# Kernel tuning notes

Hardware: AMD Instinct MI355X
Metric: run time of the kernel (lower is better)

The kernel has to match this reference:

```python
import jax, jax.numpy as jnp
import numpy as np

TEXT = 226          # text_seq_length
D = 1024            # model / inner dim
HEADS = 16
HD = D // HEADS     # 64
F = 13              # latent frames
FH, FW = 8, 12      # feature h/w = H/8/2, W/8/2
ST = F * FH * FW    # 1248 spatial tokens
S = TEXT + ST       # 1474 full sequence
NEG = -1e9


def sdpa(q, k, v, bias=None):
    # q:[b,h,Q,d] k,v:[b,h,K,d]; math path of F.scaled_dot_product_attention
    scale = 1.0 / jnp.sqrt(jnp.asarray(q.shape[-1], q.dtype))
    s = jnp.einsum('bhqd,bhkd->bhqk', q, k) * scale
    if bias is not None:
        s = s + bias
    p = jax.nn.softmax(s, axis=-1)
    return jnp.einsum('bhqk,bhkd->bhqd', p, v)


def setup_inputs() -> dict:
    key = jax.random.key(0)
    ks = jax.random.split(key, 11)
    w = 0.02
    return {
        'hidden_states': jax.random.normal(ks[0], (2, ST, D), jnp.float32),
        'encoder_hidden_states': jax.random.normal(ks[1], (2, TEXT, D), jnp.float32),
        'mask': jax.random.randint(ks[2], (F, 1, FH, FW), 0, 2),  # masks_for_attn (binary)
        'wq': jax.random.normal(ks[3], (D, D), jnp.float32) * w,
        'bq': jnp.zeros((D,), jnp.float32),
        'wk': jax.random.normal(ks[4], (D, D), jnp.float32) * w,
        'bk': jnp.zeros((D,), jnp.float32),
        'wv': jax.random.normal(ks[5], (D, D), jnp.float32) * w,
        'bv': jnp.zeros((D,), jnp.float32),
        'wo': jax.random.normal(ks[6], (D, D), jnp.float32) * w,
        'bo': jnp.zeros((D,), jnp.float32),
    }


def reference(hidden_states, encoder_hidden_states, mask, wq, bq, wk, bk, wv, bv, wo, bo):
    B = hidden_states.shape[0]  # 2: [cond, uncond]
    x = jnp.concatenate([encoder_hidden_states, hidden_states], axis=1)  # [2,S,D]

    def proj(w, b):
        y = x @ w + b                                   # [2,S,D]
        return y.reshape(B, S, HEADS, HD).transpose(0, 2, 1, 3)  # [2,H,S,hd]

    q = proj(wq, bq)
    k = proj(wk, bk)
    v = proj(wv, bv)

    # chunk into cond / uncond (source)
    key_cond, source_key = k[0:1], k[1:2]
    value_cond, source_value = v[0:1], v[1:2]

    # spatio-temporal source K/V (drop text tokens)
    st_source_key = source_key[:, :, TEXT:, :]    # [1,H,ST,hd]
    st_source_value = source_value[:, :, TEXT:, :]

    # 'masked' selective attention: the torch code gathers, per frame, the
    # source tokens where masks_for_attn > 0 and concatenates them after
    # key_cond. Softmax over a gathered subset == softmax over the full
    # appended set with -inf bias on unselected positions (identical math).
    sel = (mask[:, 0] > 0).reshape(-1)            # [ST] frame-major f,h,w order
    append_bias = jnp.where(sel, 0.0, NEG).astype(q.dtype)
    bias = jnp.concatenate([jnp.zeros((S,), q.dtype), append_bias])[None, None, None, :]  # [1,1,1,S+ST]

    st_key_cond = jnp.concatenate([key_cond, st_source_key], axis=2)      # [1,H,S+ST,hd]
    st_value_cond = jnp.concatenate([value_cond, st_source_value], axis=2)

    text_q = q[0:1, :, :TEXT, :]
    st_q = q[0:1, :, TEXT:, :]

    # extend_st_for_text_keys=True: text queries also attend to extended keys
    text_hs = sdpa(text_q, st_key_cond, st_value_cond, bias)  # [1,H,TEXT,hd]
    st_hs = sdpa(st_q, st_key_cond, st_value_cond, bias)      # [1,H,ST,hd]
    cond_hs = jnp.concatenate([text_hs, st_hs], axis=2)       # [1,H,S,hd]

    uncond_hs = sdpa(q[1:2], k[1:2], v[1:2])                  # [1,H,S,hd]

    hs = jnp.concatenate([cond_hs, uncond_hs], axis=0)        # [2,H,S,hd]
    hs = hs.transpose(0, 2, 1, 3).reshape(B, S, D)
    out = hs @ wo + bo                                        # to_out[0]; to_out[1] dropout is identity in eval

    return out[:, TEXT:, :], out[:, :TEXT, :]                 # (hidden_states, encoder_hidden_states)
```

## Files before the change

kernel.cpp:

```cpp
#include <hip/hip_runtime.h>
#include <hip/hip_bf16.h>

#define TEXT_N 226
#define D_N    1024
#define HEADS_N 16
#define HD_N   64
#define ST_N   1248
#define S_N    1474
#define L0_N   2722
#define NT_C   43
#define NT_U   24
#define BC_N   (NT_C*64)
#define SP_N   1536
#define MB_N   24
#define KB_N   16
#define NEGB2  (-1.442695e9f)
#define SCALE2 (0.125f * 1.44269504f)

typedef __hip_bfloat16 bf16_t;
typedef short s16x8 __attribute__((ext_vector_type(8)));
typedef short s16x4 __attribute__((ext_vector_type(4)));
typedef float f32x4 __attribute__((ext_vector_type(4)));

__device__ __forceinline__ f32x4 mfma16(s16x8 a, s16x8 b, f32x4 c) {
    return __builtin_amdgcn_mfma_f32_16x16x32_bf16(a, b, c, 0, 0, 0);
}

typedef __attribute__((address_space(1))) const unsigned int gu32;
typedef __attribute__((address_space(3))) unsigned int lu32;
__device__ __forceinline__ void glds16(const void* g, void* l) {
    __builtin_amdgcn_global_load_lds((gu32*)g, (lu32*)l, 16, 0, 0);
}

__device__ __forceinline__ short f2bs(float x) {
    unsigned u = __float_as_uint(x);
    u += 0x7FFF + ((u >> 16) & 1);
    return (short)(u >> 16);
}
__device__ __forceinline__ unsigned pk2(float a, float b) {
    float2 f; f.x = a; f.y = b;
    __hip_bfloat162 h = __float22bfloat162_rn(f);
    return *(unsigned*)&h;
}
__device__ __forceinline__ int swz(int r, int c) {
    return r * 64 + ((((c >> 3) ^ (r & 7)) << 3) | (c & 7));
}

__global__ __launch_bounds__(256) void prep(
    const float* __restrict__ hid, const float* __restrict__ enc,
    const int* __restrict__ mask,
    const float* __restrict__ wq, const float* __restrict__ wk,
    const float* __restrict__ wv, const float* __restrict__ wo,
    bf16_t* __restrict__ wimg, bf16_t* __restrict__ xb,
    float* __restrict__ biasc, float* __restrict__ biasu) {
    __shared__ float Lw[64 * 129];
    const int b = blockIdx.x, t = threadIdx.x;
    if (b < 512) {
        const int wid = b >> 7, nblk = (b >> 4) & 7, kb = b & 15;
        const float* w = (wid == 0) ? wq : (wid == 1) ? wk : (wid == 2) ? wv : wo;
        const int k0 = kb * 64, n0 = nblk * 128;
#pragma unroll
        for (int i = 0; i < 8; i++) {
            int idx = t + i * 256;
            int kr = idx >> 5, c4 = (idx & 31) * 4;
            float4 v = *(const float4*)(w + (size_t)(k0 + kr) * D_N + n0 + c4);
            Lw[kr * 129 + c4 + 0] = v.x; Lw[kr * 129 + c4 + 1] = v.y;
            Lw[kr * 129 + c4 + 2] = v.z; Lw[kr * 129 + c4 + 3] = v.w;
        }
        __syncthreads();
        bf16_t* dst = wimg + (((size_t)wid * 8 + nblk) * 16 + kb) * 8192;
#pragma unroll
        for (int i = 0; i < 4; i++) {
            int u = t + i * 256;
            int r = u >> 3, p = u & 7;
            int ul = p ^ (r & 7);
            s16x8 o;
#pragma unroll
            for (int e = 0; e < 8; e++)
                o[e] = f2bs(Lw[(ul * 8 + e) * 129 + r]);
            *(s16x8*)(dst + r * 64 + p * 8) = o;
        }
    } else if (b < 896) {
        const int tile = b - 512;
        const int mblk = tile >> 4, kb = tile & 15;
        bf16_t* dst = xb + (size_t)tile * 8192;
#pragma unroll
        for (int i = 0; i < 4; i++) {
            int u = t + i * 256;
            int r = u >> 3, p = u & 7;
            int m = mblk * 128 + r;
            int bb = m >= SP_N; int s = m - bb * SP_N;
            if (s >= S_N) continue;
            const float* src = (s < TEXT_N)
                ? (enc + (size_t)(bb * TEXT_N + s) * D_N)
                : (hid + (size_t)(bb * ST_N + (s - TEXT_N)) * D_N);
            int k = kb * 64 + (p ^ (r & 7)) * 8;
            float4 f0 = *(const float4*)(src + k);
            float4 f1 = *(const float4*)(src + k + 4);
            s16x8 o;
            o[0]=f2bs(f0.x); o[1]=f2bs(f0.y); o[2]=f2bs(f0.z); o[3]=f2bs(f0.w);
            o[4]=f2bs(f1.x); o[5]=f2bs(f1.y); o[6]=f2bs(f1.z); o[7]=f2bs(f1.w);
            *(s16x8*)(dst + r * 64 + p * 8) = o;
        }
    } else {
        int j = (b - 896) * 256 + t;
        if (j < BC_N) {
            float v = -8.f;
            if (j >= L0_N) v = NEGB2;
            else if (j >= S_N) v = (mask[j - S_N] > 0) ? -8.f : NEGB2;
            biasc[j] = v;
        }
        int j2 = j - BC_N;
        if (j2 >= 0 && j2 < SP_N) biasu[j2] = (j2 < S_N) ? -8.f : NEGB2;
    }
}

__global__ __launch_bounds__(256) void qkv_proj(
    const bf16_t* __restrict__ xb, const bf16_t* __restrict__ wimg,
    const float* __restrict__ bq, const float* __restrict__ bk, const float* __restrict__ bv,
    bf16_t* __restrict__ Q, bf16_t* __restrict__ Kc, bf16_t* __restrict__ Ku,
    bf16_t* __restrict__ Vc, bf16_t* __restrict__ Vu) {
    __shared__ __align__(16) bf16_t As[4096];
    __shared__ __align__(16) bf16_t Bs[8192];
    const int z = blockIdx.z;
    const float* bias = (z == 0) ? bq : (z == 1) ? bk : bv;
    const int nblk = blockIdx.x, mblk = blockIdx.y;
    const int m0 = mblk * 64;
    const int mt = mblk >> 1, rowOff = (mblk & 1) * 64;
    const int t = threadIdx.x, wave = t >> 6, lane = t & 63, ln = lane & 15, qd = lane >> 4;
    const bf16_t* Ai = xb + ((size_t)mt * KB_N) * 8192 + rowOff * 64;
    const bf16_t* Bi = wimg + ((size_t)z * 8 + nblk) * KB_N * 8192;

    f32x4 acc[8];
    const f32x4 z4 = {0.f, 0.f, 0.f, 0.f};
#pragma unroll
    for (int ni = 0; ni < 8; ni++) acc[ni] = z4;

    for (int kb = 0; kb < KB_N; kb++) {
        const bf16_t* at = Ai + (size_t)kb * 8192;
        const bf16_t* bt = Bi + (size_t)kb * 8192;
#pragma unroll
        for (int i = 0; i < 2; i++)
            glds16(at + (t + i * 256) * 8, As + (t + i * 256) * 8);
#pragma unroll
        for (int i = 0; i < 4; i++)
            glds16(bt + (t + i * 256) * 8, Bs + (t + i * 256) * 8);
        __syncthreads();
#pragma unroll
        for (int kk = 0; kk < 2; kk++) {
            const int po = (((kk * 4 + qd) ^ (ln & 7)) << 3);
            s16x8 af = *(const s16x8*)(As + (wave * 16 + ln) * 64 + po);
#pragma unroll
            for (int ni = 0; ni < 8; ni++) {
                s16x8 bfr = *(const s16x8*)(Bs + (ni * 16 + ln) * 64 + po);
                acc[ni] = mfma16(af, bfr, acc[ni]);
            }
        }
        __syncthreads();
    }

    const int b = m0 >= SP_N;
    const int sbase = m0 - b * SP_N + wave * 16 + qd * 4;
#pragma unroll
    for (int ni = 0; ni < 8; ni++) {
        int n = nblk * 128 + ni * 16 + ln;
        float bn = bias[n];
        int h = n >> 6, d = n & 63;
        int s = sbase;
        if (s >= S_N) continue;
        if (z == 2) {
            s16x4 pk;
#pragma unroll
            for (int r = 0; r < 4; r++) pk[r] = f2bs(acc[ni][r] + bn);
            bool full = (s + 3 < S_N);
            if (!b) {
                if (full) {
                    *(s16x4*)(Vc + ((size_t)h * NT_C + (s >> 6)) * 4096 + swz(d, s & 63)) = pk;
                } else {
                    for (int r = 0; r < 4; r++)
                        if (s + r < S_N)
                            *(short*)&Vc[((size_t)h * NT_C + ((s + r) >> 6)) * 4096 + swz(d, (s + r) & 63)] = pk[r];
                }
            } else {
                if (full) {
                    *(s16x4*)(Vu + ((size_t)h * NT_U + (s >> 6)) * 4096 + swz(d, s & 63)) = pk;
                    if (s >= TEXT_N) {
                        int j = s + 1248;
                        *(s16x4*)(Vc + ((size_t)h * NT_C + (j >> 6)) * 4096 + swz(d, j & 63)) = pk;
                    } else if (s + 3 >= TEXT_N) {
                        for (int r = 0; r < 4; r++)
                            if (s + r >= TEXT_N) {
                                int j = s + r + 1248;
                                *(short*)&Vc[((size_t)h * NT_C + (j >> 6)) * 4096 + swz(d, j & 63)] = pk[r];
                            }
                    }
                } else {
                    for (int r = 0; r < 4; r++)
                        if (s + r < S_N) {
                            *(short*)&Vu[((size_t)h * NT_U + ((s + r) >> 6)) * 4096 + swz(d, (s + r) & 63)] = pk[r];
                            if (s + r >= TEXT_N) {
                                int j = s + r + 1248;
                                *(short*)&Vc[((size_t)h * NT_C + (j >> 6)) * 4096 + swz(d, j & 63)] = pk[r];
                            }
                        }
                }
            }
        } else {
#pragma unroll
            for (int r = 0; r < 4; r++) {
                int sr = s + r;
                if (sr >= S_N) continue;
                short v = f2bs(acc[ni][r] + bn);
                if (z == 0) {
                    *(short*)&Q[((size_t)(b * HEADS_N + h) * SP_N + sr) * HD_N + d] = v;
                } else {
                    if (!b) {
                        *(short*)&Kc[((size_t)h * NT_C + (sr >> 6)) * 4096 + swz(sr & 63, d)] = v;
                    } else {
                        *(short*)&Ku[((size_t)h * NT_U + (sr >> 6)) * 4096 + swz(sr & 63, d)] = v;
                        if (sr >= TEXT_N) {
                            int j = sr + 1248;
                            *(short*)&Kc[((size_t)h * NT_C + (j >> 6)) * 4096 + swz(j & 63, d)] = v;
                        }
                    }
                }
            }
        }
    }
}

__global__ __launch_bounds__(256) void attn_k(
    const bf16_t* __restrict__ Q, const bf16_t* __restrict__ Kc, const bf16_t* __restrict__ Ku,
    const bf16_t* __restrict__ Vc, const bf16_t* __restrict__ Vu,
    const float* __restrict__ biasc, const float* __restrict__ biasu,
    bf16_t* __restrict__ hs) {
    __shared__ __align__(16) bf16_t Ks[4096];
    __shared__ __align__(16) bf16_t Vs[4096];
    __shared__ __align__(16) bf16_t Ps[4][1024];
    __shared__ __align__(16) float  bsL[BC_N];
    const int cs = blockIdx.z, h = blockIdx.y, q0 = blockIdx.x * 64;
    const int nt = cs ? NT_U : NT_C;
    const bf16_t* Ki = cs ? (Ku + (size_t)h * NT_U * 4096) : (Kc + (size_t)h * NT_C * 4096);
    const bf16_t* Vi = cs ? (Vu + (size_t)h * NT_U * 4096) : (Vc + (size_t)h * NT_C * 4096);
    const float* bsrc = cs ? biasu : biasc;
    const int t = threadIdx.x, wave = t >> 6, lane = t & 63, ln = lane & 15, qd = lane >> 4;
    const int q = q0 + wave * 16 + ln;

    for (int i = t * 4; i < nt * 64; i += 1024)
        *(float4*)(bsL + i) = *(const float4*)(bsrc + i);

    const bf16_t* Qp = Q + ((size_t)(cs * HEADS_N + h) * SP_N + q) * HD_N;
    s16x8 qf[2];
    qf[0] = *(const s16x8*)(Qp + qd * 8);
    qf[1] = *(const s16x8*)(Qp + 32 + qd * 8);

    f32x4 o[4];
    const f32x4 z4 = {0.f, 0.f, 0.f, 0.f};
#pragma unroll
    for (int mi = 0; mi < 4; mi++) o[mi] = z4;
    float l_r = 0.f;
    bf16_t* pw = (bf16_t*)Ps[wave];

    for (int kt = 0; kt < nt; kt++) {
        const bf16_t* kp = Ki + (size_t)kt * 4096;
        const bf16_t* vp = Vi + (size_t)kt * 4096;
#pragma unroll
        for (int i = 0; i < 2; i++) {
            glds16(kp + (t + i * 256) * 8, Ks + (t + i * 256) * 8);
            glds16(vp + (t + i * 256) * 8, Vs + (t + i * 256) * 8);
        }
        __syncthreads();

        f32x4 st[4];
#pragma unroll
        for (int ni = 0; ni < 4; ni++) st[ni] = z4;
#pragma unroll
        for (int kk = 0; kk < 2; kk++) {
            const int po = (((kk * 4 + qd) ^ (ln & 7)) << 3);
#pragma unroll
            for (int ni = 0; ni < 4; ni++) {
                s16x8 kf = *(const s16x8*)(Ks + (ni * 16 + ln) * 64 + po);
                st[ni] = mfma16(kf, qf[kk], st[ni]);
            }
        }
        float rs = 0.f;
#pragma unroll
        for (int ni = 0; ni < 4; ni++) {
            f32x4 bv4 = *(const f32x4*)(bsL + kt * 64 + ni * 16 + qd * 4);
#pragma unroll
            for (int r = 0; r < 4; r++) {
                float p = exp2f(fmaf(st[ni][r], SCALE2, bv4[r]));
                st[ni][r] = p;
                rs += p;
            }
        }
        rs += __shfl_xor(rs, 16);
        rs += __shfl_xor(rs, 32);
        l_r += rs;
#pragma unroll
        for (int ni = 0; ni < 4; ni++) {
            uint2 pk;
            pk.x = pk2(st[ni][0], st[ni][1]);
            pk.y = pk2(st[ni][2], st[ni][3]);
            int c0 = ni * 16 + qd * 4;
            *(uint2*)&pw[ln * 64 + ((((c0 >> 3) ^ (ln & 7)) << 3) | (c0 & 7))] = pk;
        }
        asm volatile("s_waitcnt lgkmcnt(0)" ::: "memory");
#pragma unroll
        for (int kk = 0; kk < 2; kk++) {
            const int po = (((kk * 4 + qd) ^ (ln & 7)) << 3);
            s16x8 pb = *(const s16x8*)(&pw[ln * 64 + po]);
#pragma unroll
            for (int mi = 0; mi < 4; mi++) {
                s16x8 vf = *(const s16x8*)(&Vs[(mi * 16 + ln) * 64 + po]);
                o[mi] = mfma16(vf, pb, o[mi]);
            }
        }
        __syncthreads();
    }
    if (q < S_N) {
        float inv = 1.f / l_r;
        int m = cs * SP_N + q;
        bf16_t* dst = hs + ((size_t)(m >> 7) * 16 + h) * 8192;
        int r = m & 127;
#pragma unroll
        for (int mi = 0; mi < 4; mi++) {
            uint2 ov;
            ov.x = pk2(o[mi][0] * inv, o[mi][1] * inv);
            ov.y = pk2(o[mi][2] * inv, o[mi][3] * inv);
            int c0 = mi * 16 + qd * 4;
            *(uint2*)&dst[r * 64 + ((((c0 >> 3) ^ (r & 7)) << 3) | (c0 & 7))] = ov;
        }
    }
}

__global__ __launch_bounds__(256) void out_proj(
    const bf16_t* __restrict__ hsi, const bf16_t* __restrict__ wimg,
    const float* __restrict__ bo, float* __restrict__ out) {
    __shared__ __align__(16) bf16_t As[4096];
    __shared__ __align__(16) bf16_t Bs[8192];
    const int nblk = blockIdx.x, mblk = blockIdx.y;
    const int m0 = mblk * 64;
    const int mt = mblk >> 1, rowOff = (mblk & 1) * 64;
    const int t = threadIdx.x, wave = t >> 6, lane = t & 63, ln = lane & 15, qd = lane >> 4;
    const bf16_t* Ai = hsi + ((size_t)mt * KB_N) * 8192 + rowOff * 64;
    const bf16_t* Bi = wimg + ((size_t)3 * 8 + nblk) * KB_N * 8192;

    f32x4 acc[8];
    const f32x4 z4 = {0.f, 0.f, 0.f, 0.f};
#pragma unroll
    for (int ni = 0; ni < 8; ni++) acc[ni] = z4;

    for (int kb = 0; kb < KB_N; kb++) {
        const bf16_t* at = Ai + (size_t)kb * 8192;
        const bf16_t* bt = Bi + (size_t)kb * 8192;
#pragma unroll
        for (int i = 0; i < 2; i++)
            glds16(at + (t + i * 256) * 8, As + (t + i * 256) * 8);
#pragma unroll
        for (int i = 0; i < 4; i++)
            glds16(bt + (t + i * 256) * 8, Bs + (t + i * 256) * 8);
        __syncthreads();
#pragma unroll
        for (int kk = 0; kk < 2; kk++) {
            const int po = (((kk * 4 + qd) ^ (ln & 7)) << 3);
            s16x8 af = *(const s16x8*)(As + (wave * 16 + ln) * 64 + po);
#pragma unroll
            for (int ni = 0; ni < 8; ni++) {
                s16x8 bfr = *(const s16x8*)(Bs + (ni * 16 + ln) * 64 + po);
                acc[ni] = mfma16(af, bfr, acc[ni]);
            }
        }
        __syncthreads();
    }
    const int b = m0 >= SP_N;
    const int sbase = m0 - b * SP_N + wave * 16 + qd * 4;
#pragma unroll
    for (int ni = 0; ni < 8; ni++) {
        int n = nblk * 128 + ni * 16 + ln;
        float bn = bo[n];
#pragma unroll
        for (int r = 0; r < 4; r++) {
            int s = sbase + r;
            if (s >= S_N) continue;
            float v = acc[ni][r] + bn;
            size_t off = (s >= TEXT_N)
                ? ((size_t)(b * ST_N + (s - TEXT_N)) * D_N + n)
                : ((size_t)2 * ST_N * D_N + (size_t)(b * TEXT_N + s) * D_N + n);
            out[off] = v;
        }
    }
}

extern "C" void kernel_launch(void* const* d_in, const int* in_sizes, int n_in,
                              void* d_out, int out_size, void* d_ws, size_t ws_size,
                              hipStream_t stream) {
    const float* hid = (const float*)d_in[0];
    const float* enc = (const float*)d_in[1];
    const int*  mask = (const int*)d_in[2];
    const float* wq = (const float*)d_in[3];
    const float* bq = (const float*)d_in[4];
    const float* wk = (const float*)d_in[5];
    const float* bk = (const float*)d_in[6];
    const float* wv = (const float*)d_in[7];
    const float* bv = (const float*)d_in[8];
    const float* wo = (const float*)d_in[9];
    const float* bo = (const float*)d_in[10];

    bf16_t* w = (bf16_t*)d_ws;
    const size_t WIMG = (size_t)4 * 8 * 16 * 8192;
    const size_t XIMG = (size_t)MB_N * KB_N * 8192;
    bf16_t* wimg = w;
    bf16_t* xb   = wimg + WIMG;
    bf16_t* Qb   = xb + XIMG;
    bf16_t* Kc   = Qb + (size_t)2 * HEADS_N * SP_N * HD_N;
    bf16_t* Ku   = Kc + (size_t)HEADS_N * NT_C * 4096;
    bf16_t* Vc   = Ku + (size_t)HEADS_N * NT_U * 4096;
    bf16_t* Vu   = Vc + (size_t)HEADS_N * NT_C * 4096;
    float*  biasc = (float*)(Vu + (size_t)HEADS_N * NT_U * 4096);
    float*  biasu = biasc + BC_N;
    bf16_t* hsi  = xb;

    prep<<<913, 256, 0, stream>>>(hid, enc, mask, wq, wk, wv, wo, wimg, xb, biasc, biasu);
    qkv_proj<<<dim3(8, 48, 3), 256, 0, stream>>>(xb, wimg, bq, bk, bv, Qb, Kc, Ku, Vc, Vu);
    attn_k<<<dim3(24, 16, 2), 256, 0, stream>>>(Qb, Kc, Ku, Vc, Vu, biasc, biasu, hsi);
    out_proj<<<dim3(8, 48), 256, 0, stream>>>(hsi, wimg, bo, (float*)d_out);
}
```

Before: 212.2 us.

## Double-buffer K/V tiles in attention and defer row-sum reduction

The attention kernel now keeps two LDS buffers for K and V. It prefetches the next 64-key tile while computing on the current one, so global-to-LDS load latency overlaps the MFMA and softmax work, and only one barrier is needed per iteration. The per-tile cross-lane shuffle reduction of the softmax denominator moves to a single reduction after the loop. The cost is twice the LDS used for K/V, which may lower the number of resident blocks per CU.

```diff
diff --git a/kernel.cpp b/kernel.cpp
--- a/kernel.cpp
+++ b/kernel.cpp
@@ -234,8 +234,8 @@
     const bf16_t* __restrict__ Vc, const bf16_t* __restrict__ Vu,
     const float* __restrict__ biasc, const float* __restrict__ biasu,
     bf16_t* __restrict__ hs) {
-    __shared__ __align__(16) bf16_t Ks[4096];
-    __shared__ __align__(16) bf16_t Vs[4096];
+    __shared__ __align__(16) bf16_t Ks[2][4096];
+    __shared__ __align__(16) bf16_t Vs[2][4096];
     __shared__ __align__(16) bf16_t Ps[4][1024];
     __shared__ __align__(16) float  bsL[BC_N];
     const int cs = blockIdx.z, h = blockIdx.y, q0 = blockIdx.x * 64;
@@ -258,18 +258,27 @@
     const f32x4 z4 = {0.f, 0.f, 0.f, 0.f};
 #pragma unroll
     for (int mi = 0; mi < 4; mi++) o[mi] = z4;
-    float l_r = 0.f;
+    float l_p = 0.f;
     bf16_t* pw = (bf16_t*)Ps[wave];
 
+#pragma unroll
+    for (int i = 0; i < 2; i++) {
+        glds16(Ki + (t + i * 256) * 8, &Ks[0][(t + i * 256) * 8]);
+        glds16(Vi + (t + i * 256) * 8, &Vs[0][(t + i * 256) * 8]);
+    }
+
     for (int kt = 0; kt < nt; kt++) {
-        const bf16_t* kp = Ki + (size_t)kt * 4096;
-        const bf16_t* vp = Vi + (size_t)kt * 4096;
-#pragma unroll
-        for (int i = 0; i < 2; i++) {
-            glds16(kp + (t + i * 256) * 8, Ks + (t + i * 256) * 8);
-            glds16(vp + (t + i * 256) * 8, Vs + (t + i * 256) * 8);
-        }
-        __syncthreads();
+        const int buf = kt & 1;
+        __syncthreads();
+        if (kt + 1 < nt) {
+            const bf16_t* kp = Ki + (size_t)(kt + 1) * 4096;
+            const bf16_t* vp = Vi + (size_t)(kt + 1) * 4096;
+#pragma unroll
+            for (int i = 0; i < 2; i++) {
+                glds16(kp + (t + i * 256) * 8, &Ks[buf ^ 1][(t + i * 256) * 8]);
+                glds16(vp + (t + i * 256) * 8, &Vs[buf ^ 1][(t + i * 256) * 8]);
+            }
+        }
 
         f32x4 st[4];
 #pragma unroll
@@ -279,11 +288,10 @@
             const int po = (((kk * 4 + qd) ^ (ln & 7)) << 3);
 #pragma unroll
             for (int ni = 0; ni < 4; ni++) {
-                s16x8 kf = *(const s16x8*)(Ks + (ni * 16 + ln) * 64 + po);
+                s16x8 kf = *(const s16x8*)(&Ks[buf][(ni * 16 + ln) * 64 + po]);
                 st[ni] = mfma16(kf, qf[kk], st[ni]);
             }
         }
-        float rs = 0.f;
 #pragma unroll
         for (int ni = 0; ni < 4; ni++) {
             f32x4 bv4 = *(const f32x4*)(bsL + kt * 64 + ni * 16 + qd * 4);
@@ -291,12 +299,9 @@
             for (int r = 0; r < 4; r++) {
                 float p = exp2f(fmaf(st[ni][r], SCALE2, bv4[r]));
                 st[ni][r] = p;
-                rs += p;
-            }
-        }
-        rs += __shfl_xor(rs, 16);
-        rs += __shfl_xor(rs, 32);
-        l_r += rs;
+                l_p += p;
+            }
+        }
 #pragma unroll
         for (int ni = 0; ni < 4; ni++) {
             uint2 pk;
@@ -312,12 +317,14 @@
             s16x8 pb = *(const s16x8*)(&pw[ln * 64 + po]);
 #pragma unroll
             for (int mi = 0; mi < 4; mi++) {
-                s16x8 vf = *(const s16x8*)(&Vs[(mi * 16 + ln) * 64 + po]);
+                s16x8 vf = *(const s16x8*)(&Vs[buf][(mi * 16 + ln) * 64 + po]);
                 o[mi] = mfma16(vf, pb, o[mi]);
             }
         }
-        __syncthreads();
-    }
+    }
+    float l_r = l_p;
+    l_r += __shfl_xor(l_r, 16);
+    l_r += __shfl_xor(l_r, 32);
     if (q < S_N) {
         float inv = 1.f / l_r;
         int m = cs * SP_N + q;
```

Measured after the change: 201.4 us. -5.1%, faster.

## Split attention key range into two partial blocks with fp16 partials and reduction

Applied to the files above, without the earlier changes.

The attention kernel now splits each query tile's key tiles into two halves, launched as separate blocks. This doubles the grid so more of the GPU's compute units stay busy. Each half writes an unnormalised fp16 partial output and a float row sum, and a new attn_red kernel adds the two halves, normalises, and writes the swizzled bf16 layout. The bias is no longer staged in LDS: tiles below 23 use a constant -8 offset and later tiles read the bias directly from global memory. The trade-offs are an extra launch, extra global traffic for the partials, and fp16 range or precision risk in the partial sums.

```diff
diff --git a/kernel.cpp b/kernel.cpp
--- a/kernel.cpp
+++ b/kernel.cpp
@@ -1,5 +1,6 @@
 #include <hip/hip_runtime.h>
 #include <hip/hip_bf16.h>
+#include <hip/hip_fp16.h>
 
 #define TEXT_N 226
 #define D_N    1024
@@ -36,11 +37,6 @@
     unsigned u = __float_as_uint(x);
     u += 0x7FFF + ((u >> 16) & 1);
     return (short)(u >> 16);
-}
-__device__ __forceinline__ unsigned pk2(float a, float b) {
-    float2 f; f.x = a; f.y = b;
-    __hip_bfloat162 h = __float22bfloat162_rn(f);
-    return *(unsigned*)&h;
 }
 __device__ __forceinline__ int swz(int r, int c) {
     return r * 64 + ((((c >> 3) ^ (r & 7)) << 3) | (c & 7));
@@ -229,26 +225,27 @@
     }
 }
 
-__global__ __launch_bounds__(256) void attn_k(
+__global__ __launch_bounds__(256, 6) void attn_k(
     const bf16_t* __restrict__ Q, const bf16_t* __restrict__ Kc, const bf16_t* __restrict__ Ku,
     const bf16_t* __restrict__ Vc, const bf16_t* __restrict__ Vu,
     const float* __restrict__ biasc, const float* __restrict__ biasu,
-    bf16_t* __restrict__ hs) {
+    __half* __restrict__ Opart, float* __restrict__ Lpart) {
     __shared__ __align__(16) bf16_t Ks[4096];
     __shared__ __align__(16) bf16_t Vs[4096];
     __shared__ __align__(16) bf16_t Ps[4][1024];
-    __shared__ __align__(16) float  bsL[BC_N];
-    const int cs = blockIdx.z, h = blockIdx.y, q0 = blockIdx.x * 64;
+    const int qt = blockIdx.x, h = blockIdx.y, z = blockIdx.z;
+    const int cs = z >> 1, sp = z & 1;
+    const int q0 = qt * 64;
     const int nt = cs ? NT_U : NT_C;
+    const int half = (nt + 1) >> 1;
+    const int kt0 = sp ? half : 0;
+    const int kt1 = sp ? nt : half;
     const bf16_t* Ki = cs ? (Ku + (size_t)h * NT_U * 4096) : (Kc + (size_t)h * NT_C * 4096);
     const bf16_t* Vi = cs ? (Vu + (size_t)h * NT_U * 4096) : (Vc + (size_t)h * NT_C * 4096);
     const float* bsrc = cs ? biasu : biasc;
     const int t = threadIdx.x, wave = t >> 6, lane = t & 63, ln = lane & 15, qd = lane >> 4;
     const int q = q0 + wave * 16 + ln;
 
-    for (int i = t * 4; i < nt * 64; i += 1024)
-        *(float4*)(bsL + i) = *(const float4*)(bsrc + i);
-
     const bf16_t* Qp = Q + ((size_t)(cs * HEADS_N + h) * SP_N + q) * HD_N;
     s16x8 qf[2];
     qf[0] = *(const s16x8*)(Qp + qd * 8);
@@ -258,10 +255,10 @@
     const f32x4 z4 = {0.f, 0.f, 0.f, 0.f};
 #pragma unroll
     for (int mi = 0; mi < 4; mi++) o[mi] = z4;
-    float l_r = 0.f;
+    f32x4 l4 = z4;
     bf16_t* pw = (bf16_t*)Ps[wave];
 
-    for (int kt = 0; kt < nt; kt++) {
+    for (int kt = kt0; kt < kt1; kt++) {
         const bf16_t* kp = Ki + (size_t)kt * 4096;
         const bf16_t* vp = Vi + (size_t)kt * 4096;
 #pragma unroll
@@ -271,6 +268,17 @@
         }
         __syncthreads();
 
+        f32x4 bv[4];
+        if (kt >= 23) {
+#pragma unroll
+            for (int ni = 0; ni < 4; ni++)
+                bv[ni] = *(const f32x4*)(bsrc + kt * 64 + ni * 16 + qd * 4);
+        } else {
+            const f32x4 m8 = {-8.f, -8.f, -8.f, -8.f};
+#pragma unroll
+            for (int ni = 0; ni < 4; ni++) bv[ni] = m8;
+        }
+
         f32x4 st[4];
 #pragma unroll
         for (int ni = 0; ni < 4; ni++) st[ni] = z4;
@@ -283,25 +291,26 @@
                 st[ni] = mfma16(kf, qf[kk], st[ni]);
             }
         }
-        float rs = 0.f;
 #pragma unroll
         for (int ni = 0; ni < 4; ni++) {
-            f32x4 bv4 = *(const f32x4*)(bsL + kt * 64 + ni * 16 + qd * 4);
-#pragma unroll
-            for (int r = 0; r < 4; r++) {
-                float p = exp2f(fmaf(st[ni][r], SCALE2, bv4[r]));
-                st[ni][r] = p;
-                rs += p;
-            }
-        }
-        rs += __shfl_xor(rs, 16);
-        rs += __shfl_xor(rs, 32);
-        l_r += rs;
+            f32x4 s = st[ni] * SCALE2 + bv[ni];
+            f32x4 p;
+            p[0] = exp2f(s[0]); p[1] = exp2f(s[1]);
+            p[2] = exp2f(s[2]); p[3] = exp2f(s[3]);
+            st[ni] = p;
+            l4 += p;
+        }
 #pragma unroll
         for (int ni = 0; ni < 4; ni++) {
             uint2 pk;
-            pk.x = pk2(st[ni][0], st[ni][1]);
-            pk.y = pk2(st[ni][2], st[ni][3]);
+            {
+                float2 f; f.x = st[ni][0]; f.y = st[ni][1];
+                __hip_bfloat162 hh = __float22bfloat162_rn(f);
+                pk.x = *(unsigned*)&hh;
+                f.x = st[ni][2]; f.y = st[ni][3];
+                hh = __float22bfloat162_rn(f);
+                pk.y = *(unsigned*)&hh;
+            }
             int c0 = ni * 16 + qd * 4;
             *(uint2*)&pw[ln * 64 + ((((c0 >> 3) ^ (ln & 7)) << 3) | (c0 & 7))] = pk;
         }
@@ -318,19 +327,55 @@
         }
         __syncthreads();
     }
-    if (q < S_N) {
-        float inv = 1.f / l_r;
-        int m = cs * SP_N + q;
-        bf16_t* dst = hs + ((size_t)(m >> 7) * 16 + h) * 8192;
-        int r = m & 127;
-#pragma unroll
-        for (int mi = 0; mi < 4; mi++) {
-            uint2 ov;
-            ov.x = pk2(o[mi][0] * inv, o[mi][1] * inv);
-            ov.y = pk2(o[mi][2] * inv, o[mi][3] * inv);
-            int c0 = mi * 16 + qd * 4;
-            *(uint2*)&dst[r * 64 + ((((c0 >> 3) ^ (r & 7)) << 3) | (c0 & 7))] = ov;
-        }
+
+    const int tix = ((cs * 16 + h) * 24 + qt) * 2 + sp;
+    __half* op = Opart + (size_t)tix * 4096;
+#pragma unroll
+    for (int mi = 0; mi < 4; mi++) {
+        int c0 = mi * 16 + qd * 4;
+        float2 f0; f0.x = o[mi][0]; f0.y = o[mi][1];
+        float2 f1; f1.x = o[mi][2]; f1.y = o[mi][3];
+        __half2 h0 = __float22half2_rn(f0);
+        __half2 h1 = __float22half2_rn(f1);
+        uint2 u; u.x = *(unsigned*)&h0; u.y = *(unsigned*)&h1;
+        *(uint2*)(op + (wave * 16 + ln) * 64 + c0) = u;
+    }
+    float l_r = (l4[0] + l4[1]) + (l4[2] + l4[3]);
+    l_r += __shfl_xor(l_r, 16);
+    l_r += __shfl_xor(l_r, 32);
+    if (qd == 0) Lpart[(size_t)tix * 64 + wave * 16 + ln] = l_r;
+}
+
+__global__ __launch_bounds__(256) void attn_red(
+    const __half* __restrict__ Opart, const float* __restrict__ Lpart,
+    bf16_t* __restrict__ hs) {
+    __shared__ float linv[64];
+    const int qt = blockIdx.x, h = blockIdx.y, cs = blockIdx.z;
+    const int base = ((cs * 16 + h) * 24 + qt) * 2;
+    const __half* p0 = Opart + (size_t)base * 4096;
+    const __half* p1 = p0 + 4096;
+    const int t = threadIdx.x;
+    if (t < 64) linv[t] = 1.f / (Lpart[(size_t)base * 64 + t] + Lpart[(size_t)(base + 1) * 64 + t]);
+    __syncthreads();
+    const int q = t >> 2, c0 = (t & 3) * 16;
+    const int m = cs * SP_N + qt * 64 + q;
+    const float inv = linv[q];
+    bf16_t* dst = hs + ((size_t)(m >> 7) * 16 + h) * 8192;
+    const int r = m & 127;
+#pragma unroll
+    for (int hh = 0; hh < 2; hh++) {
+        int c = c0 + hh * 8;
+        const __half2* a2 = (const __half2*)(p0 + q * 64 + c);
+        const __half2* b2 = (const __half2*)(p1 + q * 64 + c);
+        s16x8 o8;
+#pragma unroll
+        for (int e = 0; e < 4; e++) {
+            float2 fa = __half22float2(a2[e]);
+            float2 fb = __half22float2(b2[e]);
+            o8[2 * e]     = f2bs((fa.x + fb.x) * inv);
+            o8[2 * e + 1] = f2bs((fa.y + fb.y) * inv);
+        }
+        *(s16x8*)(dst + r * 64 + (((c >> 3) ^ (r & 7)) << 3)) = o8;
     }
 }
 
@@ -419,10 +464,13 @@
     bf16_t* Vu   = Vc + (size_t)HEADS_N * NT_C * 4096;
     float*  biasc = (float*)(Vu + (size_t)HEADS_N * NT_U * 4096);
     float*  biasu = biasc + BC_N;
+    __half* Opart = (__half*)(biasu + SP_N);
+    float*  Lpart = (float*)(Opart + (size_t)1536 * 4096);
     bf16_t* hsi  = xb;
 
     prep<<<913, 256, 0, stream>>>(hid, enc, mask, wq, wk, wv, wo, wimg, xb, biasc, biasu);
     qkv_proj<<<dim3(8, 48, 3), 256, 0, stream>>>(xb, wimg, bq, bk, bv, Qb, Kc, Ku, Vc, Vu);
-    attn_k<<<dim3(24, 16, 2), 256, 0, stream>>>(Qb, Kc, Ku, Vc, Vu, biasc, biasu, hsi);
+    attn_k<<<dim3(24, 16, 4), 256, 0, stream>>>(Qb, Kc, Ku, Vc, Vu, biasc, biasu, Opart, Lpart);
+    attn_red<<<dim3(24, 16, 2), 256, 0, stream>>>(Opart, Lpart, hsi);
     out_proj<<<dim3(8, 48), 256, 0, stream>>>(hsi, wimg, bo, (float*)d_out);
 }
```

Measured after the change: 191.2 us. 1.11x faster.
